# Kernel optimization log

Measured on AMD Instinct MI355X. Metric: run time of the kernel, lower is better.

The kernel has to match this reference:

```python
import jax, jax.numpy as jnp
import numpy as np

B, N, C, H = 2, 2048, 256, 8
HD = C // H
EPS = 1e-5


def _cdist(a, b):
    # a: (B,N,D), b: (B,M,D) -> (B,N,M) euclidean distance (torch.cdist p=2)
    d2 = (jnp.sum(a * a, -1)[:, :, None] + jnp.sum(b * b, -1)[:, None, :]
          - 2.0 * jnp.einsum('bnd,bmd->bnm', a, b))
    return jnp.sqrt(jnp.maximum(d2, 0.0))


def _ln(x, g, b):
    # LayerNorm over last axis
    m = jnp.mean(x, -1, keepdims=True)
    v = jnp.var(x, -1, keepdims=True)
    return (x - m) / jnp.sqrt(v + EPS) * g + b


def _conv1d(x, w, b=None):
    # 1x1 Conv1d: x (B,Cin,N), w (Cout,Cin)
    y = jnp.einsum('oc,bcn->bon', w, x)
    return y if b is None else y + b[:, None]


def setup_inputs() -> dict:
    key = jax.random.key(0)
    ks = jax.random.split(key, 32)
    s = 0.05
    inp = {
        'xyz_A': jax.random.normal(ks[0], (B, N, 3), jnp.float32),
        'featA': jax.random.normal(ks[1], (B, C, N), jnp.float32),
        'xyz_B': jax.random.normal(ks[2], (B, N, 3), jnp.float32),
        'featB': jax.random.normal(ks[3], (B, C, N), jnp.float32),
        # q/k/v projections (Conv1d 1x1)
        'qw': jax.random.normal(ks[4], (C, C), jnp.float32) * s,
        'qb': jnp.zeros((C,), jnp.float32),
        'kw': jax.random.normal(ks[5], (C, C), jnp.float32) * s,
        'kb': jnp.zeros((C,), jnp.float32),
        'vw': jax.random.normal(ks[6], (C, C), jnp.float32) * s,
        'vb': jnp.zeros((C,), jnp.float32),
        # spatial_bias_mlp: Conv2d(1,H/2,1,bias=False) -> BN2d(eval) -> ReLU -> Conv2d(H/2,H,1)
        'sbw1': jax.random.normal(ks[7], (H // 2,), jnp.float32) * s,
        'sbg': jnp.ones((H // 2,), jnp.float32),
        'sbb': jnp.zeros((H // 2,), jnp.float32),
        'sbm': jax.random.normal(ks[8], (H // 2,), jnp.float32) * 0.1,
        'sbv': jax.random.uniform(ks[9], (H // 2,), jnp.float32, 0.5, 1.5),
        'sbw2': jax.random.normal(ks[10], (H, H // 2), jnp.float32) * s,
        'sbb2': jnp.zeros((H,), jnp.float32),
        # dissimilarity projections
        'qdw': jax.random.normal(ks[11], (C, C), jnp.float32) * s,
        'qdb': jnp.zeros((C,), jnp.float32),
        'kdw': jax.random.normal(ks[12], (C, C), jnp.float32) * s,
        'kdb': jnp.zeros((C,), jnp.float32),
        # LayerNorms
        'lin_g': jnp.ones((C,), jnp.float32), 'lin_b': jnp.zeros((C,), jnp.float32),
        'lsim_g': jnp.ones((C,), jnp.float32), 'lsim_b': jnp.zeros((C,), jnp.float32),
        'ldis_g': jnp.ones((C,), jnp.float32), 'ldis_b': jnp.zeros((C,), jnp.float32),
        # fusion MLP: Conv1d(3C,2C,bias=False) -> BN1d(eval) -> ReLU -> Dropout(eval) -> Conv1d(2C,C)
        'fw1': jax.random.normal(ks[13], (2 * C, 3 * C), jnp.float32) * s,
        'fbg': jnp.ones((2 * C,), jnp.float32),
        'fbb': jnp.zeros((2 * C,), jnp.float32),
        'fbm': jax.random.normal(ks[14], (2 * C,), jnp.float32) * 0.1,
        'fbv': jax.random.uniform(ks[15], (2 * C,), jnp.float32, 0.5, 1.5),
        'fw2': jax.random.normal(ks[16], (C, 2 * C), jnp.float32) * s,
        'fb2': jnp.zeros((C,), jnp.float32),
    }
    return inp


def _forward(xyz_A, featA, xyz_B, featB, qw, qb, kw, kb, vw, vb,
             sbw1, sbg, sbb, sbm, sbv, sbw2, sbb2,
             qdw, qdb, kdw, kdb,
             lin_g, lin_b, lsim_g, lsim_b, ldis_g, ldis_b,
             fw1, fbg, fbb, fbm, fbv, fw2, fb2):
    # Pre-norm of featA over channels
    featA_norm = _ln(featA.transpose(0, 2, 1), lin_g, lin_b).transpose(0, 2, 1)  # (B,C,N)

    # Spatial bias: -cdist -> 1x1 conv (in_ch=1) -> BN(eval) -> ReLU -> 1x1 conv
    dist = _cdist(xyz_A, xyz_B)                                # (B,N,N)
    t = jnp.einsum('o,bnm->bonm', sbw1, -dist)                 # (B,H/2,N,N)
    t = (t - sbm[:, None, None]) / jnp.sqrt(sbv + EPS)[:, None, None]
    t = t * sbg[:, None, None] + sbb[:, None, None]
    t = jax.nn.relu(t)
    spatial_bias = jnp.einsum('oh,bhnm->bonm', sbw2, t) + sbb2[:, None, None]  # (B,H,N,N)

    # Similarity path
    q = _conv1d(featA_norm, qw, qb).reshape(B, H, HD, N).transpose(0, 1, 3, 2)  # (B,H,N,hd)
    k = _conv1d(featB, kw, kb).reshape(B, H, HD, N).transpose(0, 1, 3, 2)
    sim_scores = jnp.einsum('bhnd,bhmd->bhnm', q, k) / (HD ** 0.5) + spatial_bias

    # Dissimilarity path: feature cdist + spatial bias
    qd = _conv1d(featA_norm, qdw, qdb).transpose(0, 2, 1)      # (B,N,C)
    kd = _conv1d(featB, kdw, kdb).transpose(0, 2, 1)
    dissim_scores = _cdist(qd, kd)[:, None] + spatial_bias     # (B,H,N,N)

    sim_w = jax.nn.softmax(sim_scores, -1)
    dis_w = jax.nn.softmax(dissim_scores, -1)

    v = _conv1d(featB, vw, vb).reshape(B, H, HD, N).transpose(0, 1, 3, 2)       # (B,H,N,hd)
    ctx_sim = jnp.einsum('bhnm,bhmd->bhnd', sim_w, v).transpose(0, 1, 3, 2).reshape(B, C, N)
    ctx_sim = _ln(ctx_sim.transpose(0, 2, 1), lsim_g, lsim_b).transpose(0, 2, 1)
    ctx_dis = jnp.einsum('bhnm,bhmd->bhnd', dis_w, v).transpose(0, 1, 3, 2).reshape(B, C, N)
    ctx_dis = _ln(ctx_dis.transpose(0, 2, 1), ldis_g, ldis_b).transpose(0, 2, 1)

    fused = jnp.concatenate([featA_norm, ctx_sim, ctx_dis], axis=1)            # (B,3C,N)
    x = jnp.einsum('oc,bcn->bon', fw1, fused)
    x = (x - fbm[:, None]) / jnp.sqrt(fbv + EPS)[:, None] * fbg[:, None] + fbb[:, None]
    x = jax.nn.relu(x)  # Dropout is identity in eval mode
    out = _conv1d(x, fw2, fb2) + featA  # residual_proj is Identity (in==out)
    return out


def reference(xyz_A, featA, xyz_B, featB, qw, qb, kw, kb, vw, vb,
              sbw1, sbg, sbb, sbm, sbv, sbw2, sbb2,
              qdw, qdb, kdw, kdb,
              lin_g, lin_b, lsim_g, lsim_b, ldis_g, ldis_b,
              fw1, fbg, fbb, fbm, fbv, fw2, fb2):
    return _forward(xyz_A, featA, xyz_B, featB, qw, qb, kw, kb, vw, vb,
                    sbw1, sbg, sbb, sbm, sbv, sbw2, sbb2,
                    qdw, qdb, kdw, kdb,
                    lin_g, lin_b, lsim_g, lsim_b, ldis_g, ldis_b,
                    fw1, fbg, fbb, fbm, fbv, fw2, fb2)
```

## Files before the change

### kernel.cpp

```cpp
#include <hip/hip_runtime.h>

#define B_ 2
#define N_ 2048
#define C_ 256
#define H_ 8
#define HD_ 32
#define EPSf 1e-5f

typedef __bf16   bf16x8 __attribute__((ext_vector_type(8)));
typedef float    f32x4  __attribute__((ext_vector_type(4)));
typedef _Float16 f16x8  __attribute__((ext_vector_type(8)));
typedef _Float16 f16x4  __attribute__((ext_vector_type(4)));
typedef _Float16 f16x2  __attribute__((ext_vector_type(2)));

static constexpr size_t MB_ = 1024 * 1024;
static constexpr size_t OFF_FANT = 0;
static constexpr size_t OFF_FBT  = 2 * MB_;
static constexpr size_t OFF_QPK  = 4 * MB_;
static constexpr size_t OFF_KPK  = 6 * MB_;
static constexpr size_t OFF_VPK  = 8 * MB_;
static constexpr size_t OFF_QDT  = 10 * MB_;
static constexpr size_t OFF_KDT  = 12 * MB_;
static constexpr size_t OFF_QQ   = 14 * MB_;
static constexpr size_t OFF_KK   = 14 * MB_ + 16 * 1024;
static constexpr size_t OFF_FDH  = 14 * MB_ + 64 * 1024;
static constexpr size_t OFF_FSD  = 14 * MB_ + 64 * 1024;
static constexpr size_t OFF_CTXS = 31 * MB_;
static constexpr size_t OFF_CTXD = 35 * MB_;
static constexpr size_t OFF_CSLN = 39 * MB_;
static constexpr size_t OFF_CDLN = 41 * MB_;
static constexpr size_t OFF_X1T  = 43 * MB_;
static constexpr size_t WS_NEED  = 47 * MB_;
static constexpr size_t OFF2_PART  = 47 * MB_;
static constexpr size_t OFF2_STATM = 55 * MB_;
static constexpr size_t OFF2_STATL = 56 * MB_;
static constexpr size_t OFF2_CSLN  = 15 * MB_;
static constexpr size_t OFF2_CDLN  = 17 * MB_;
static constexpr size_t OFF2_X1T   = 19 * MB_;
static constexpr size_t WS_NEED2   = 63 * MB_;

__device__ __forceinline__ float rfl(float x){
  return __uint_as_float(__builtin_amdgcn_readfirstlane(__float_as_uint(x)));
}
__device__ __forceinline__ bf16x8 cvt8(const float* p){
  float4 a = *reinterpret_cast<const float4*>(p);
  float4 c = *reinterpret_cast<const float4*>(p + 4);
  bf16x8 r;
  r[0]=(__bf16)a.x; r[1]=(__bf16)a.y; r[2]=(__bf16)a.z; r[3]=(__bf16)a.w;
  r[4]=(__bf16)c.x; r[5]=(__bf16)c.y; r[6]=(__bf16)c.z; r[7]=(__bf16)c.w;
  return r;
}
__device__ __forceinline__ unsigned int packh2(float lo, float hi){
  f16x2 h; h[0] = (_Float16)lo; h[1] = (_Float16)hi;
  return __builtin_bit_cast(unsigned int, h);
}
__device__ __forceinline__ void unpackh2(unsigned int u, float& lo, float& hi){
  f16x2 h = __builtin_bit_cast(f16x2, u);
  lo = (float)h[0]; hi = (float)h[1];
}

__global__ __launch_bounds__(256) void lnA_pack(const float* __restrict__ featA,
    __bf16* __restrict__ fanT, const float* __restrict__ gam, const float* __restrict__ bet){
  int b = blockIdx.y, n0 = blockIdx.x * 32;
  int t = threadIdx.x, nl = t & 31, cg = t >> 5;
  __shared__ float tile[256][33];
  __shared__ float red1[8][32], red2[8][32], mus[32], rss[32];
  __shared__ float gsh[256], bsh[256];
  gsh[t] = gam[t]; bsh[t] = bet[t];
  #pragma unroll
  for (int i = 0; i < 32; i++){
    int c = cg * 32 + i;
    tile[c][nl] = featA[((size_t)(b * C_ + c)) * N_ + n0 + nl];
  }
  __syncthreads();
  float s1 = 0.f, s2 = 0.f;
  #pragma unroll
  for (int i = 0; i < 32; i++){
    float v = tile[cg * 32 + i][nl];
    s1 += v; s2 += v * v;
  }
  red1[cg][nl] = s1; red2[cg][nl] = s2;
  __syncthreads();
  if (t < 32){
    float a = 0.f, q = 0.f;
    #pragma unroll
    for (int i = 0; i < 8; i++){ a += red1[i][t]; q += red2[i][t]; }
    float m = a / (float)C_;
    mus[t] = m; rss[t] = rsqrtf(q / (float)C_ - m * m + EPSf);
  }
  __syncthreads();
  float mu = mus[nl], rs = rss[nl];
  size_t obase = ((size_t)(b * N_ + n0 + nl)) * C_;
  #pragma unroll
  for (int i = 0; i < 32; i++){
    int c = cg * 32 + i;
    fanT[obase + c] = (__bf16)((tile[c][nl] - mu) * rs * gsh[c] + bsh[c]);
  }
}

__global__ __launch_bounds__(256) void packT_kernel(const float* __restrict__ featB,
    __bf16* __restrict__ fbT){
  int b = blockIdx.z, c0 = blockIdx.y * 64, n0 = blockIdx.x * 64;
  int t = threadIdx.x;
  __shared__ float tile[64][65];
  int cl = t >> 6, nl = t & 63;
  #pragma unroll
  for (int i = 0; i < 16; i++)
    tile[i * 4 + cl][nl] = featB[((size_t)(b * C_ + c0 + i * 4 + cl)) * N_ + n0 + nl];
  __syncthreads();
  int nr = t >> 2, cc = (t & 3) * 16;
  alignas(16) __bf16 tmp[16];
  #pragma unroll
  for (int j = 0; j < 16; j++) tmp[j] = (__bf16)tile[cc + j][nr];
  size_t d = ((size_t)(b * N_ + n0 + nr)) * C_ + c0 + cc;
  *reinterpret_cast<uint4*>(&fbT[d])     = *reinterpret_cast<uint4*>(&tmp[0]);
  *reinterpret_cast<uint4*>(&fbT[d + 8]) = *reinterpret_cast<uint4*>(&tmp[8]);
}

__global__ __launch_bounds__(256) void proj_mfma(const __bf16* __restrict__ fanT,
    const __bf16* __restrict__ fbT, __bf16* __restrict__ wsh, int vfp16,
    const float* __restrict__ qw, const float* __restrict__ qb,
    const float* __restrict__ kw, const float* __restrict__ kb,
    const float* __restrict__ vw, const float* __restrict__ vb,
    const float* __restrict__ qdw, const float* __restrict__ qdb,
    const float* __restrict__ kdw, const float* __restrict__ kdb){
  const int p = blockIdx.z % 5, b = blockIdx.z / 5;
  const int t = threadIdx.x, w = t >> 6, lane = t & 63, ln = lane & 15, g = lane >> 4;
  const float *W, *bias;
  const __bf16* X;
  __bf16* Y;
  if (p == 0)      { W = qw;  bias = qb;  X = fanT; Y = wsh + (OFF_QPK - OFF_FANT) / 2; }
  else if (p == 1) { W = kw;  bias = kb;  X = fbT;  Y = wsh + (OFF_KPK - OFF_FANT) / 2; }
  else if (p == 2) { W = vw;  bias = vb;  X = fbT;  Y = wsh + (OFF_VPK - OFF_FANT) / 2; }
  else if (p == 3) { W = qdw; bias = qdb; X = fanT; Y = wsh + (OFF_QDT - OFF_FANT) / 2; }
  else             { W = kdw; bias = kdb; X = fbT;  Y = wsh + (OFF_KDT - OFF_FANT) / 2; }

  f32x4 acc[4];
  #pragma unroll
  for (int i = 0; i < 4; i++) acc[i] = (f32x4){0.f, 0.f, 0.f, 0.f};

  if (p != 2){
    const int n0w = blockIdx.x * 64 + w * 16, o0 = blockIdx.y * 64;
    #pragma unroll
    for (int ks = 0; ks < 8; ks++){
      bf16x8 af = *reinterpret_cast<const bf16x8*>(
          &X[((size_t)(b * N_ + n0w + ln)) * C_ + ks * 32 + g * 8]);
      #pragma unroll
      for (int ot = 0; ot < 4; ot++){
        bf16x8 bf = cvt8(&W[(size_t)(o0 + ot * 16 + ln) * C_ + ks * 32 + g * 8]);
        acc[ot] = __builtin_amdgcn_mfma_f32_16x16x32_bf16(af, bf, acc[ot], 0, 0, 0);
      }
    }
    const float inv = 0.17677669529663687f;
    #pragma unroll
    for (int ot = 0; ot < 4; ot++){
      int o = o0 + ot * 16 + ln;
      float bz = bias[o];
      #pragma unroll
      for (int r = 0; r < 4; r++){
        int n = n0w + g * 4 + r;
        float val = acc[ot][r] + bz;
        if (p == 0){
          val *= inv;
          Y[(((size_t)(b * H_ + (o >> 5))) * N_ + n) * HD_ + (o & 31)] = (__bf16)val;
        } else if (p == 1){
          Y[(((size_t)(b * H_ + (o >> 5))) * N_ + n) * HD_ + (o & 31)] = (__bf16)val;
        } else {
          Y[((size_t)(b * N_ + n)) * C_ + o] = (__bf16)val;
        }
      }
    }
  } else {
    const int o0w = blockIdx.y * 64 + w * 16, n0 = blockIdx.x * 64;
    #pragma unroll
    for (int ks = 0; ks < 8; ks++){
      bf16x8 af = cvt8(&W[(size_t)(o0w + ln) * C_ + ks * 32 + g * 8]);
      #pragma unroll
      for (int nt = 0; nt < 4; nt++){
        bf16x8 bf = *reinterpret_cast<const bf16x8*>(
            &X[((size_t)(b * N_ + n0 + nt * 16 + ln)) * C_ + ks * 32 + g * 8]);
        acc[nt] = __builtin_amdgcn_mfma_f32_16x16x32_bf16(af, bf, acc[nt], 0, 0, 0);
      }
    }
    float bz[4];
    #pragma unroll
    for (int r = 0; r < 4; r++) bz[r] = vb[o0w + g * 4 + r];
    #pragma unroll
    for (int nt = 0; nt < 4; nt++)
      #pragma unroll
      for (int r = 0; r < 4; r++){
        int o = o0w + g * 4 + r, n = n0 + nt * 16 + ln;
        size_t idx = ((size_t)(b * C_ + o)) * N_ + n;
        float val = acc[nt][r] + bz[r];
        if (vfp16) ((_Float16*)Y)[idx] = (_Float16)val;
        else       Y[idx] = (__bf16)val;
      }
  }
}

__global__ __launch_bounds__(256) void norms_b(const __bf16* __restrict__ qdT,
    const __bf16* __restrict__ kdT, float* __restrict__ qq, float* __restrict__ kk){
  int b = blockIdx.y, n = blockIdx.x * 64 + (threadIdx.x >> 2), part = threadIdx.x & 3;
  size_t base = ((size_t)(b * N_ + n)) * C_ + part * 64;
  float s1 = 0.f, s2 = 0.f;
  #pragma unroll
  for (int i = 0; i < 8; i++){
    bf16x8 a = *reinterpret_cast<const bf16x8*>(&qdT[base + i * 8]);
    bf16x8 d = *reinterpret_cast<const bf16x8*>(&kdT[base + i * 8]);
    #pragma unroll
    for (int j = 0; j < 8; j++){
      float fa = (float)a[j]; s1 += fa * fa;
      float fd = (float)d[j]; s2 += fd * fd;
    }
  }
  s1 += __shfl_xor(s1, 1); s1 += __shfl_xor(s1, 2);
  s2 += __shfl_xor(s2, 1); s2 += __shfl_xor(s2, 2);
  if (part == 0){ qq[b * N_ + n] = s1; kk[b * N_ + n] = s2; }
}

__global__ __launch_bounds__(256) void pairdist_mfma(const __bf16* __restrict__ qdT,
    const __bf16* __restrict__ kdT, const float* __restrict__ qq,
    const float* __restrict__ kk, const float* __restrict__ xyzA,
    const float* __restrict__ xyzB, unsigned int* __restrict__ fsd){
  const int t = threadIdx.x, w = t >> 6, lane = t & 63, ln = lane & 15, g = lane >> 4;
  const int b = blockIdx.z, n0 = blockIdx.y * 64, n0w = n0 + w * 16, m0 = blockIdx.x * 64;
  __shared__ float4 xa[64], xb[64];
  __shared__ unsigned int sbl[4][16][68];

  if (t < 64){
    const float* p = &xyzA[((size_t)(b * N_ + n0 + t)) * 3];
    xa[t] = make_float4(p[0], p[1], p[2], 0.f);
  } else if (t < 128){
    const float* p = &xyzB[((size_t)(b * N_ + m0 + t - 64)) * 3];
    xb[t - 64] = make_float4(p[0], p[1], p[2], 0.f);
  }
  bf16x8 qfr[8];
  #pragma unroll
  for (int ks = 0; ks < 8; ks++)
    qfr[ks] = *reinterpret_cast<const bf16x8*>(
        &qdT[((size_t)(b * N_ + n0w + ln)) * C_ + ks * 32 + g * 8]);
  float qqv[4];
  #pragma unroll
  for (int r = 0; r < 4; r++) qqv[r] = qq[b * N_ + n0w + g * 4 + r];
  __syncthreads();
  float4 xav[4];
  #pragma unroll
  for (int r = 0; r < 4; r++) xav[r] = xa[w * 16 + g * 4 + r];

  #pragma unroll
  for (int mt = 0; mt < 4; mt++){
    f32x4 a = (f32x4){0.f, 0.f, 0.f, 0.f};
    #pragma unroll
    for (int ks = 0; ks < 8; ks++){
      bf16x8 kfr = *reinterpret_cast<const bf16x8*>(
          &kdT[((size_t)(b * N_ + m0 + mt * 16 + ln)) * C_ + ks * 32 + g * 8]);
      a = __builtin_amdgcn_mfma_f32_16x16x32_bf16(qfr[ks], kfr, a, 0, 0, 0);
    }
    float kkv = kk[b * N_ + m0 + mt * 16 + ln];
    float4 xbv = xb[mt * 16 + ln];
    #pragma unroll
    for (int r = 0; r < 4; r++){
      float d2 = qqv[r] + kkv - 2.f * a[r];
      float fd = sqrtf(fmaxf(d2, 0.f));
      float dx = xav[r].x - xbv.x, dy = xav[r].y - xbv.y, dz = xav[r].z - xbv.z;
      float sd = sqrtf(dx * dx + dy * dy + dz * dz);
      sbl[w][g * 4 + r][mt * 16 + ln] = packh2(fd, sd);
    }
  }
  #pragma unroll
  for (int it = 0; it < 4; it++){
    int row = it * 4 + (lane >> 4), cq = lane & 15;
    uint4 v = *reinterpret_cast<const uint4*>(&sbl[w][row][cq * 4]);
    *reinterpret_cast<uint4*>(&fsd[((size_t)(b * N_ + n0w + row)) * N_ + m0 + cq * 4]) = v;
  }
}

struct TileRegs { uint4 fu[4]; bf16x8 kf[4]; };

__device__ __forceinline__ void load_tile(TileRegs& T, const __bf16* kbase,
    const unsigned int* fsdrow, int m0, int ln, int g){
  #pragma unroll
  for (int mt = 0; mt < 4; mt++){
    T.fu[mt] = *reinterpret_cast<const uint4*>(&fsdrow[m0 + mt * 16 + g * 4]);
    T.kf[mt] = *reinterpret_cast<const bf16x8*>(&kbase[(size_t)(m0 + mt * 16 + ln) * HD_ + g * 8]);
  }
}

__device__ __forceinline__ void compute_tile(const TileRegs& T,
    const _Float16* vbase, int m0, int ln, int g, bf16x8 qf,
    const float* Ac, const float* Bc, const float* W2h, float C0,
    f32x4* os, f32x4* od, float& ms, float& ls, float& md, float& ld){
  f32x4 sa[4];
  #pragma unroll
  for (int mt = 0; mt < 4; mt++){
    f32x4 z = (f32x4){0.f, 0.f, 0.f, 0.f};
    sa[mt] = __builtin_amdgcn_mfma_f32_16x16x32_bf16(T.kf[mt], qf, z, 0, 0, 0);
  }
  f16x4 vf[2][4];
  #pragma unroll
  for (int mt = 0; mt < 4; mt++)
    #pragma unroll
    for (int dt = 0; dt < 2; dt++)
      vf[dt][mt] = *reinterpret_cast<const f16x4*>(
          &vbase[(size_t)(dt * 16 + ln) * N_ + m0 + mt * 16 + g * 4]);
  f32x4 dvv[4];
  float mxs = -3e38f, mxd = -3e38f;
  #pragma unroll
  for (int mt = 0; mt < 4; mt++){
    #pragma unroll
    for (int r = 0; r < 4; r++){
      unsigned int uu = (r == 0) ? T.fu[mt].x : (r == 1) ? T.fu[mt].y
                      : (r == 2) ? T.fu[mt].z : T.fu[mt].w;
      float fd, sd;
      unpackh2(uu, fd, sd);
      float u0 = fmaxf(fmaf(Ac[0], sd, Bc[0]), 0.f);
      float u1 = fmaxf(fmaf(Ac[1], sd, Bc[1]), 0.f);
      float u2 = fmaxf(fmaf(Ac[2], sd, Bc[2]), 0.f);
      float u3 = fmaxf(fmaf(Ac[3], sd, Bc[3]), 0.f);
      float bias = C0 + W2h[0] * u0 + W2h[1] * u1 + W2h[2] * u2 + W2h[3] * u3;
      float s = sa[mt][r] + bias;
      float d = fd + bias;
      sa[mt][r] = s; dvv[mt][r] = d;
      mxs = fmaxf(mxs, s); mxd = fmaxf(mxd, d);
    }
  }
  mxs = fmaxf(mxs, __shfl_xor(mxs, 16)); mxs = fmaxf(mxs, __shfl_xor(mxs, 32));
  mxd = fmaxf(mxd, __shfl_xor(mxd, 16)); mxd = fmaxf(mxd, __shfl_xor(mxd, 32));
  float nms = fmaxf(ms, mxs), als = __expf(ms - nms);
  float nmd = fmaxf(md, mxd), ald = __expf(md - nmd);
  f16x4 pAs[4], pAd[4];
  float pss = 0.f, psd = 0.f;
  #pragma unroll
  for (int mt = 0; mt < 4; mt++)
    #pragma unroll
    for (int r = 0; r < 4; r++){
      float pv = __expf(sa[mt][r] - nms); pss += pv; pAs[mt][r] = (_Float16)pv;
      float qv = __expf(dvv[mt][r] - nmd); psd += qv; pAd[mt][r] = (_Float16)qv;
    }
  pss += __shfl_xor(pss, 16); pss += __shfl_xor(pss, 32);
  psd += __shfl_xor(psd, 16); psd += __shfl_xor(psd, 32);
  ls = ls * als + pss; ms = nms;
  ld = ld * ald + psd; md = nmd;
  float alsr[4], aldr[4];
  #pragma unroll
  for (int r = 0; r < 4; r++){
    alsr[r] = __shfl(als, g * 4 + r);
    aldr[r] = __shfl(ald, g * 4 + r);
  }
  #pragma unroll
  for (int dt = 0; dt < 2; dt++)
    #pragma unroll
    for (int r = 0; r < 4; r++){ os[dt][r] *= alsr[r]; od[dt][r] *= aldr[r]; }
  #pragma unroll
  for (int mt = 0; mt < 4; mt++)
    #pragma unroll
    for (int dt = 0; dt < 2; dt++){
      os[dt] = __builtin_amdgcn_mfma_f32_16x16x16f16(pAs[mt], vf[dt][mt], os[dt], 0, 0, 0);
      od[dt] = __builtin_amdgcn_mfma_f32_16x16x16f16(pAd[mt], vf[dt][mt], od[dt], 0, 0, 0);
    }
}

__global__ __launch_bounds__(256) void dual_attn3(
    const __bf16* __restrict__ qpk, const __bf16* __restrict__ kpk,
    const _Float16* __restrict__ vph, const unsigned int* __restrict__ fsd,
    const float* __restrict__ sbw1, const float* __restrict__ sbg, const float* __restrict__ sbb,
    const float* __restrict__ sbm, const float* __restrict__ sbv,
    const float* __restrict__ sbw2, const float* __restrict__ sbb2,
    _Float16* __restrict__ partO, float* __restrict__ statM, float* __restrict__ statL){
  const int t = threadIdx.x, w = t >> 6, lane = t & 63, ln = lane & 15, g = lane >> 4;
  const int h = blockIdx.y;
  const int b = blockIdx.z >> 1, split = blockIdx.z & 1;
  const int nbase = blockIdx.x * 64 + w * 16;
  const int n = nbase + ln;
  const int mstart = split * (N_ / 2);

  float Ac[4], Bc[4], W2h[4];
  #pragma unroll
  for (int j = 0; j < 4; j++){
    float rs = rsqrtf(sbv[j] + EPSf);
    Ac[j]  = rfl(-sbw1[j] * rs * sbg[j]);
    Bc[j]  = rfl(-sbm[j] * rs * sbg[j] + sbb[j]);
    W2h[j] = rfl(sbw2[h * 4 + j]);
  }
  float C0 = rfl(sbb2[h]);

  bf16x8 qf = *reinterpret_cast<const bf16x8*>(
      &qpk[(((size_t)(b * H_ + h)) * N_ + n) * HD_ + g * 8]);
  const unsigned int* fsdrow = &fsd[((size_t)(b * N_ + n)) * N_];
  const __bf16* kbase = &kpk[(((size_t)(b * H_ + h)) * N_) * HD_];
  const _Float16* vbase = &vph[((size_t)(b * C_ + h * HD_)) * N_];

  f32x4 os[2], od[2];
  #pragma unroll
  for (int i = 0; i < 2; i++){ os[i] = (f32x4){0.f,0.f,0.f,0.f}; od[i] = (f32x4){0.f,0.f,0.f,0.f}; }
  float ms = -3e38f, ls = 0.f, md = -3e38f, ld = 0.f;

  TileRegs TA, TB;
  load_tile(TA, kbase, fsdrow, mstart, ln, g);
  for (int i = 0; i < 16; i += 2){
    int m0 = mstart + i * 64;
    load_tile(TB, kbase, fsdrow, m0 + 64, ln, g);
    compute_tile(TA, vbase, m0, ln, g, qf, Ac, Bc, W2h, C0, os, od, ms, ls, md, ld);
    if (i + 2 < 16) load_tile(TA, kbase, fsdrow, m0 + 128, ln, g);
    compute_tile(TB, vbase, m0 + 64, ln, g, qf, Ac, Bc, W2h, C0, os, od, ms, ls, md, ld);
  }

  float is = 1.f / ls, idd = 1.f / ld;
  float isr[4], idr[4];
  #pragma unroll
  for (int r = 0; r < 4; r++){
    isr[r] = __shfl(is, g * 4 + r);
    idr[r] = __shfl(idd, g * 4 + r);
  }
  #pragma unroll
  for (int dt = 0; dt < 2; dt++)
    #pragma unroll
    for (int r = 0; r < 4; r++){
      int nn = nbase + g * 4 + r;
      int ch = h * HD_ + dt * 16 + ln;
      size_t p0 = (((size_t)(0 * 2 + split) * B_ + b) * N_ + nn) * C_ + ch;
      size_t p1 = (((size_t)(2 + split) * B_ + b) * N_ + nn) * C_ + ch;
      partO[p0] = (_Float16)(os[dt][r] * isr[r]);
      partO[p1] = (_Float16)(od[dt][r] * idr[r]);
    }
  if (lane < 16){
    int nn = nbase + lane;
    size_t s0 = (((size_t)(0 * 2 + split) * B_ + b) * H_ + h) * N_ + nn;
    size_t s1 = (((size_t)(2 + split) * B_ + b) * H_ + h) * N_ + nn;
    statM[s0] = ms; statL[s0] = ls;
    statM[s1] = md; statL[s1] = ld;
  }
}

__global__ __launch_bounds__(256) void combine_ln(
    const _Float16* __restrict__ partO, const float* __restrict__ statM,
    const float* __restrict__ statL, __bf16* __restrict__ csLN, __bf16* __restrict__ cdLN,
    const float* __restrict__ lsg, const float* __restrict__ lsb,
    const float* __restrict__ ldg, const float* __restrict__ ldb){
  const int path = blockIdx.y;
  const int w = threadIdx.x >> 6, lane = threadIdx.x & 63;
  const size_t row = (size_t)blockIdx.x * 4 + w;
  const int b = (int)(row >> 11), n = (int)(row & (N_ - 1));
  const int h = lane >> 3;
  const float* gg = path ? ldg : lsg;
  const float* bb = path ? ldb : lsb;
  __bf16* dst = path ? cdLN : csLN;

  size_t pb0 = (((size_t)(path * 2 + 0) * B_ + b) * N_ + n) * C_ + lane * 4;
  size_t pb1 = (((size_t)(path * 2 + 1) * B_ + b) * N_ + n) * C_ + lane * 4;
  f16x4 p0 = *reinterpret_cast<const f16x4*>(&partO[pb0]);
  f16x4 p1 = *reinterpret_cast<const f16x4*>(&partO[pb1]);
  size_t sb0 = (((size_t)(path * 2 + 0) * B_ + b) * H_ + h) * N_ + n;
  size_t sb1 = (((size_t)(path * 2 + 1) * B_ + b) * H_ + h) * N_ + n;
  float m0 = statM[sb0], l0 = statL[sb0];
  float m1 = statM[sb1], l1 = statL[sb1];
  float M = fmaxf(m0, m1);
  float w0 = l0 * __expf(m0 - M), w1 = l1 * __expf(m1 - M);
  float inv = 1.f / (w0 + w1);
  float o[4];
  #pragma unroll
  for (int j = 0; j < 4; j++)
    o[j] = (w0 * (float)p0[j] + w1 * (float)p1[j]) * inv;

  float s1 = o[0] + o[1] + o[2] + o[3];
  float s2 = o[0]*o[0] + o[1]*o[1] + o[2]*o[2] + o[3]*o[3];
  #pragma unroll
  for (int off = 1; off < 64; off <<= 1){
    s1 += __shfl_xor(s1, off);
    s2 += __shfl_xor(s2, off);
  }
  float mu = s1 / (float)C_;
  float rs = rsqrtf(s2 / (float)C_ - mu * mu + EPSf);
  float4 g4 = *reinterpret_cast<const float4*>(&gg[lane * 4]);
  float4 b4 = *reinterpret_cast<const float4*>(&bb[lane * 4]);
  alignas(8) __bf16 o4[4];
  o4[0] = (__bf16)((o[0] - mu) * rs * g4.x + b4.x);
  o4[1] = (__bf16)((o[1] - mu) * rs * g4.y + b4.y);
  o4[2] = (__bf16)((o[2] - mu) * rs * g4.z + b4.z);
  o4[3] = (__bf16)((o[3] - mu) * rs * g4.w + b4.w);
  *reinterpret_cast<uint2*>(&dst[row * C_ + lane * 4]) = *reinterpret_cast<uint2*>(o4);
}

__global__ __launch_bounds__(256) void fdist_mfma(const __bf16* __restrict__ qdT,
    const __bf16* __restrict__ kdT, const float* __restrict__ qq,
    const float* __restrict__ kk, _Float16* __restrict__ fdh){
  const int t = threadIdx.x, w = t >> 6, lane = t & 63, ln = lane & 15, g = lane >> 4;
  const int b = blockIdx.z, n0 = blockIdx.y * 64 + w * 16, m0 = blockIdx.x * 64;
  __shared__ _Float16 sbl[4][16][68];

  bf16x8 qfr[8];
  #pragma unroll
  for (int ks = 0; ks < 8; ks++)
    qfr[ks] = *reinterpret_cast<const bf16x8*>(
        &qdT[((size_t)(b * N_ + n0 + ln)) * C_ + ks * 32 + g * 8]);
  float qqv[4];
  #pragma unroll
  for (int r = 0; r < 4; r++) qqv[r] = qq[b * N_ + n0 + g * 4 + r];

  #pragma unroll
  for (int mt = 0; mt < 4; mt++){
    f32x4 a = (f32x4){0.f, 0.f, 0.f, 0.f};
    #pragma unroll
    for (int ks = 0; ks < 8; ks++){
      bf16x8 kfr = *reinterpret_cast<const bf16x8*>(
          &kdT[((size_t)(b * N_ + m0 + mt * 16 + ln)) * C_ + ks * 32 + g * 8]);
      a = __builtin_amdgcn_mfma_f32_16x16x32_bf16(qfr[ks], kfr, a, 0, 0, 0);
    }
    float kkv = kk[b * N_ + m0 + mt * 16 + ln];
    #pragma unroll
    for (int r = 0; r < 4; r++){
      float d2 = qqv[r] + kkv - 2.f * a[r];
      sbl[w][g * 4 + r][mt * 16 + ln] = (_Float16)sqrtf(fmaxf(d2, 0.f));
    }
  }
  __syncthreads();
  #pragma unroll
  for (int it = 0; it < 8; it++){
    int row = (lane >> 5) + it * 2, colu = lane & 31;
    unsigned int u = *reinterpret_cast<const unsigned int*>(&sbl[w][row][colu * 2]);
    *reinterpret_cast<unsigned int*>(&fdh[((size_t)(b * N_ + n0 + row)) * N_ + m0 + colu * 2]) = u;
  }
}

__global__ __launch_bounds__(256) void dual_attn(
    const __bf16* __restrict__ qpk, const __bf16* __restrict__ kpk, const __bf16* __restrict__ vpk,
    const _Float16* __restrict__ fdh,
    const float* __restrict__ xyzA, const float* __restrict__ xyzB,
    const float* __restrict__ sbw1, const float* __restrict__ sbg, const float* __restrict__ sbb,
    const float* __restrict__ sbm, const float* __restrict__ sbv,
    const float* __restrict__ sbw2, const float* __restrict__ sbb2,
    float* __restrict__ ctxsT, float* __restrict__ ctxdT){
  const int t = threadIdx.x, w = t >> 6, lane = t & 63, ln = lane & 15, g = lane >> 4;
  const int h = blockIdx.y, b = blockIdx.z;
  const int nbase = blockIdx.x * 64 + w * 16;
  const int n = nbase + ln;

  float Ac[4], Bc[4], W2h[4];
  #pragma unroll
  for (int j = 0; j < 4; j++){
    float rs = rsqrtf(sbv[j] + EPSf);
    Ac[j]  = rfl(-sbw1[j] * rs * sbg[j]);
    Bc[j]  = rfl(-sbm[j] * rs * sbg[j] + sbb[j]);
    W2h[j] = rfl(sbw2[h * 4 + j]);
  }
  float C0 = rfl(sbb2[h]);

  bf16x8 qf = *reinterpret_cast<const bf16x8*>(
      &qpk[(((size_t)(b * H_ + h)) * N_ + n) * HD_ + g * 8]);
  float ax = xyzA[((size_t)(b * N_ + n)) * 3 + 0];
  float ay = xyzA[((size_t)(b * N_ + n)) * 3 + 1];
  float az = xyzA[((size_t)(b * N_ + n)) * 3 + 2];
  const _Float16* fdrow = &fdh[((size_t)(b * N_ + n)) * N_];

  f32x4 os[2], od[2];
  #pragma unroll
  for (int i = 0; i < 2; i++){ os[i] = (f32x4){0.f,0.f,0.f,0.f}; od[i] = (f32x4){0.f,0.f,0.f,0.f}; }
  float ms = -3e38f, ls = 0.f, md = -3e38f, ld = 0.f;

  __shared__ __align__(16) float ss[4][16][68];
  __shared__ float4 xbb[4][64];

  for (int m0 = 0; m0 < N_; m0 += 64){
    __syncthreads();
    {
      const float* xp = &xyzB[((size_t)(b * N_ + m0 + lane)) * 3];
      xbb[w][lane] = make_float4(xp[0], xp[1], xp[2], 0.f);
    }
    f32x4 sa[4];
    #pragma unroll
    for (int i = 0; i < 4; i++) sa[i] = (f32x4){0.f, 0.f, 0.f, 0.f};
    #pragma unroll
    for (int mt = 0; mt < 4; mt++){
      bf16x8 kf = *reinterpret_cast<const bf16x8*>(
          &kpk[(((size_t)(b * H_ + h)) * N_ + m0 + mt * 16 + ln) * HD_ + g * 8]);
      sa[mt] = __builtin_amdgcn_mfma_f32_16x16x32_bf16(qf, kf, sa[mt], 0, 0, 0);
    }
    #pragma unroll
    for (int mt = 0; mt < 4; mt++)
      #pragma unroll
      for (int r = 0; r < 4; r++)
        ss[w][g * 4 + r][mt * 16 + ln] = sa[mt][r];
    __syncthreads();

    #pragma unroll
    for (int kh = 0; kh < 2; kh++){
      float s8[8], d8[8];
      {
        float4 A4 = *reinterpret_cast<const float4*>(&ss[w][ln][kh * 32 + g * 8]);
        float4 B4 = *reinterpret_cast<const float4*>(&ss[w][ln][kh * 32 + g * 8 + 4]);
        s8[0]=A4.x; s8[1]=A4.y; s8[2]=A4.z; s8[3]=A4.w;
        s8[4]=B4.x; s8[5]=B4.y; s8[6]=B4.z; s8[7]=B4.w;
      }
      f16x8 fv = *reinterpret_cast<const f16x8*>(&fdrow[m0 + kh * 32 + g * 8]);
      float mxs = -3e38f, mxd = -3e38f;
      #pragma unroll
      for (int j = 0; j < 8; j++){
        float4 xk = xbb[w][kh * 32 + g * 8 + j];
        float dx = ax - xk.x, dy = ay - xk.y, dz = az - xk.z;
        float sd = sqrtf(dx * dx + dy * dy + dz * dz);
        float bias = C0;
        #pragma unroll
        for (int u = 0; u < 4; u++)
          bias += W2h[u] * fmaxf(fmaf(Ac[u], sd, Bc[u]), 0.f);
        s8[j] += bias;
        d8[j] = (float)fv[j] + bias;
        mxs = fmaxf(mxs, s8[j]);
        mxd = fmaxf(mxd, d8[j]);
      }
      mxs = fmaxf(mxs, __shfl_xor(mxs, 16)); mxs = fmaxf(mxs, __shfl_xor(mxs, 32));
      mxd = fmaxf(mxd, __shfl_xor(mxd, 16)); mxd = fmaxf(mxd, __shfl_xor(mxd, 32));
      float nms = fmaxf(ms, mxs), als = __expf(ms - nms);
      float nmd = fmaxf(md, mxd), ald = __expf(md - nmd);
      float pss = 0.f, psd = 0.f;
      bf16x8 pfs, pfd;
      #pragma unroll
      for (int j = 0; j < 8; j++){
        float pv = __expf(s8[j] - nms); pss += pv; pfs[j] = (__bf16)pv;
        float qv = __expf(d8[j] - nmd); psd += qv; pfd[j] = (__bf16)qv;
      }
      pss += __shfl_xor(pss, 16); pss += __shfl_xor(pss, 32);
      psd += __shfl_xor(psd, 16); psd += __shfl_xor(psd, 32);
      ls = ls * als + pss; ms = nms;
      ld = ld * ald + psd; md = nmd;
      os[0] *= als; os[1] *= als; od[0] *= ald; od[1] *= ald;
      #pragma unroll
      for (int dt = 0; dt < 2; dt++){
        bf16x8 vf = *reinterpret_cast<const bf16x8*>(
            &vpk[((size_t)(b * C_ + h * HD_ + dt * 16 + ln)) * N_ + m0 + kh * 32 + g * 8]);
        os[dt] = __builtin_amdgcn_mfma_f32_16x16x32_bf16(vf, pfs, os[dt], 0, 0, 0);
        od[dt] = __builtin_amdgcn_mfma_f32_16x16x32_bf16(vf, pfd, od[dt], 0, 0, 0);
      }
    }
  }
  float is = 1.f / ls, idv = 1.f / ld;
  #pragma unroll
  for (int dt = 0; dt < 2; dt++)
    #pragma unroll
    for (int r = 0; r < 4; r++){
      int ch = h * HD_ + dt * 16 + g * 4 + r;
      size_t base = ((size_t)(b * N_ + n)) * C_ + ch;
      ctxsT[base] = os[dt][r] * is;
      ctxdT[base] = od[dt][r] * idv;
    }
}

__global__ __launch_bounds__(256) void ln_ctx(const float* __restrict__ ctxsT,
    const float* __restrict__ ctxdT, __bf16* __restrict__ csLN, __bf16* __restrict__ cdLN,
    const float* __restrict__ lsg, const float* __restrict__ lsb,
    const float* __restrict__ ldg, const float* __restrict__ ldb){
  const float* src = blockIdx.y ? ctxdT : ctxsT;
  __bf16* dst = blockIdx.y ? cdLN : csLN;
  const float* gg = blockIdx.y ? ldg : lsg;
  const float* bb = blockIdx.y ? ldb : lsb;
  int w = threadIdx.x >> 6, lane = threadIdx.x & 63;
  size_t row = (size_t)blockIdx.x * 4 + w;
  float4 v = *reinterpret_cast<const float4*>(&src[row * C_ + lane * 4]);
  float s1 = v.x + v.y + v.z + v.w;
  float s2 = v.x * v.x + v.y * v.y + v.z * v.z + v.w * v.w;
  #pragma unroll
  for (int off = 1; off < 64; off <<= 1){
    s1 += __shfl_xor(s1, off);
    s2 += __shfl_xor(s2, off);
  }
  float m = s1 / (float)C_;
  float rs = rsqrtf(s2 / (float)C_ - m * m + EPSf);
  float4 g4 = *reinterpret_cast<const float4*>(&gg[lane * 4]);
  float4 b4 = *reinterpret_cast<const float4*>(&bb[lane * 4]);
  alignas(8) __bf16 o4[4];
  o4[0] = (__bf16)((v.x - m) * rs * g4.x + b4.x);
  o4[1] = (__bf16)((v.y - m) * rs * g4.y + b4.y);
  o4[2] = (__bf16)((v.z - m) * rs * g4.z + b4.z);
  o4[3] = (__bf16)((v.w - m) * rs * g4.w + b4.w);
  *reinterpret_cast<uint2*>(&dst[row * C_ + lane * 4]) = *reinterpret_cast<uint2*>(o4);
}

__global__ __launch_bounds__(256) void fusion1_mfma(const __bf16* __restrict__ fanT,
    const __bf16* __restrict__ csLN, const __bf16* __restrict__ cdLN,
    __bf16* __restrict__ X1T, const float* __restrict__ fw1,
    const float* __restrict__ fbg, const float* __restrict__ fbb,
    const float* __restrict__ fbm, const float* __restrict__ fbv){
  const int t = threadIdx.x, w = t >> 6, lane = t & 63, ln = lane & 15, g = lane >> 4;
  const int b = blockIdx.z, o0 = blockIdx.y * 64, n0w = blockIdx.x * 64 + w * 16;
  f32x4 acc[4];
  #pragma unroll
  for (int i = 0; i < 4; i++) acc[i] = (f32x4){0.f, 0.f, 0.f, 0.f};
  const __bf16* segs[3] = {fanT, csLN, cdLN};
  #pragma unroll
  for (int ks = 0; ks < 24; ks++){
    const __bf16* base = segs[ks >> 3];
    int coff = (ks & 7) * 32 + g * 8;
    bf16x8 af = *reinterpret_cast<const bf16x8*>(
        &base[((size_t)(b * N_ + n0w + ln)) * C_ + coff]);
    #pragma unroll
    for (int ot = 0; ot < 4; ot++){
      bf16x8 bf = cvt8(&fw1[(size_t)(o0 + ot * 16 + ln) * (3 * C_) + ks * 32 + g * 8]);
      acc[ot] = __builtin_amdgcn_mfma_f32_16x16x32_bf16(af, bf, acc[ot], 0, 0, 0);
    }
  }
  #pragma unroll
  for (int ot = 0; ot < 4; ot++){
    int o = o0 + ot * 16 + ln;
    float mn = fbm[o], rs = rsqrtf(fbv[o] + EPSf), gg = fbg[o], be = fbb[o];
    #pragma unroll
    for (int r = 0; r < 4; r++){
      int n = n0w + g * 4 + r;
      float x = (acc[ot][r] - mn) * rs * gg + be;
      X1T[((size_t)(b * N_ + n)) * (2 * C_) + o] = (__bf16)fmaxf(x, 0.f);
    }
  }
}

__global__ __launch_bounds__(256) void fusion2_mfma(const __bf16* __restrict__ X1T,
    const float* __restrict__ fw2, const float* __restrict__ fb2,
    const float* __restrict__ featA, float* __restrict__ out){
  const int t = threadIdx.x, w = t >> 6, lane = t & 63, ln = lane & 15, g = lane >> 4;
  const int b = blockIdx.z, o0w = blockIdx.y * 64 + w * 16, n0 = blockIdx.x * 64;
  f32x4 acc[4];
  #pragma unroll
  for (int i = 0; i < 4; i++) acc[i] = (f32x4){0.f, 0.f, 0.f, 0.f};
  #pragma unroll
  for (int ks = 0; ks < 16; ks++){
    bf16x8 af = cvt8(&fw2[(size_t)(o0w + ln) * (2 * C_) + ks * 32 + g * 8]);
    #pragma unroll
    for (int nt = 0; nt < 4; nt++){
      bf16x8 bf = *reinterpret_cast<const bf16x8*>(
          &X1T[((size_t)(b * N_ + n0 + nt * 16 + ln)) * (2 * C_) + ks * 32 + g * 8]);
      acc[nt] = __builtin_amdgcn_mfma_f32_16x16x32_bf16(af, bf, acc[nt], 0, 0, 0);
    }
  }
  float bz[4];
  #pragma unroll
  for (int r = 0; r < 4; r++) bz[r] = fb2[o0w + g * 4 + r];
  #pragma unroll
  for (int nt = 0; nt < 4; nt++)
    #pragma unroll
    for (int r = 0; r < 4; r++){
      int o = o0w + g * 4 + r, n = n0 + nt * 16 + ln;
      size_t oi = ((size_t)(b * C_ + o)) * N_ + n;
      out[oi] = acc[nt][r] + bz[r] + featA[oi];
    }
}

extern "C" void kernel_launch(void* const* d_in, const int* in_sizes, int n_in,
                              void* d_out, int out_size, void* d_ws, size_t ws_size,
                              hipStream_t stream){
  (void)in_sizes; (void)n_in; (void)out_size;
  if (ws_size < WS_NEED) return;

  const float* xyzA  = (const float*)d_in[0];
  const float* featA = (const float*)d_in[1];
  const float* xyzB  = (const float*)d_in[2];
  const float* featB = (const float*)d_in[3];
  const float* qw  = (const float*)d_in[4];   const float* qb  = (const float*)d_in[5];
  const float* kw  = (const float*)d_in[6];   const float* kb  = (const float*)d_in[7];
  const float* vw  = (const float*)d_in[8];   const float* vb  = (const float*)d_in[9];
  const float* sbw1= (const float*)d_in[10];  const float* sbg = (const float*)d_in[11];
  const float* sbb = (const float*)d_in[12];  const float* sbm = (const float*)d_in[13];
  const float* sbv = (const float*)d_in[14];  const float* sbw2= (const float*)d_in[15];
  const float* sbb2= (const float*)d_in[16];
  const float* qdw = (const float*)d_in[17];  const float* qdb = (const float*)d_in[18];
  const float* kdw = (const float*)d_in[19];  const float* kdb = (const float*)d_in[20];
  const float* ling= (const float*)d_in[21];  const float* linb= (const float*)d_in[22];
  const float* lsg = (const float*)d_in[23];  const float* lsb = (const float*)d_in[24];
  const float* ldg = (const float*)d_in[25];  const float* ldb = (const float*)d_in[26];
  const float* fw1 = (const float*)d_in[27];  const float* fbg = (const float*)d_in[28];
  const float* fbb = (const float*)d_in[29];  const float* fbm = (const float*)d_in[30];
  const float* fbv = (const float*)d_in[31];  const float* fw2 = (const float*)d_in[32];
  const float* fb2 = (const float*)d_in[33];

  char* ws = (char*)d_ws;
  __bf16*   fanT = (__bf16*)(ws + OFF_FANT);
  __bf16*   fbT  = (__bf16*)(ws + OFF_FBT);
  __bf16*   qpk  = (__bf16*)(ws + OFF_QPK);
  __bf16*   kpk  = (__bf16*)(ws + OFF_KPK);
  __bf16*   qdT  = (__bf16*)(ws + OFF_QDT);
  __bf16*   kdT  = (__bf16*)(ws + OFF_KDT);
  float*    qq   = (float*)(ws + OFF_QQ);
  float*    kk   = (float*)(ws + OFF_KK);
  float*    out  = (float*)d_out;

  bool big = (ws_size >= WS_NEED2);

  lnA_pack<<<dim3(N_ / 32, B_), 256, 0, stream>>>(featA, fanT, ling, linb);
  packT_kernel<<<dim3(N_ / 64, C_ / 64, B_), 256, 0, stream>>>(featB, fbT);
  proj_mfma<<<dim3(N_ / 64, C_ / 64, 5 * B_), 256, 0, stream>>>(
      fanT, fbT, fanT, big ? 1 : 0, qw, qb, kw, kb, vw, vb, qdw, qdb, kdw, kdb);
  norms_b<<<dim3(N_ / 64, B_), 256, 0, stream>>>(qdT, kdT, qq, kk);

  if (big){
    _Float16*     vph  = (_Float16*)(ws + OFF_VPK);
    unsigned int* fsd  = (unsigned int*)(ws + OFF_FSD);
    _Float16* partO = (_Float16*)(ws + OFF2_PART);
    float*    statM = (float*)(ws + OFF2_STATM);
    float*    statL = (float*)(ws + OFF2_STATL);
    __bf16*   csLN  = (__bf16*)(ws + OFF2_CSLN);
    __bf16*   cdLN  = (__bf16*)(ws + OFF2_CDLN);
    __bf16*   X1T   = (__bf16*)(ws + OFF2_X1T);
    pairdist_mfma<<<dim3(N_ / 64, N_ / 64, B_), 256, 0, stream>>>(
        qdT, kdT, qq, kk, xyzA, xyzB, fsd);
    dual_attn3<<<dim3(N_ / 64, H_, B_ * 2), 256, 0, stream>>>(
        qpk, kpk, vph, fsd, sbw1, sbg, sbb, sbm, sbv, sbw2, sbb2,
        partO, statM, statL);
    combine_ln<<<dim3(B_ * N_ / 4, 2), 256, 0, stream>>>(
        partO, statM, statL, csLN, cdLN, lsg, lsb, ldg, ldb);
    fusion1_mfma<<<dim3(N_ / 64, (2 * C_) / 64, B_), 256, 0, stream>>>(
        fanT, csLN, cdLN, X1T, fw1, fbg, fbb, fbm, fbv);
    fusion2_mfma<<<dim3(N_ / 64, C_ / 64, B_), 256, 0, stream>>>(
        X1T, fw2, fb2, featA, out);
  } else {
    __bf16*   vpk  = (__bf16*)(ws + OFF_VPK);
    _Float16* fdh  = (_Float16*)(ws + OFF_FDH);
    float*  ctxsT = (float*)(ws + OFF_CTXS);
    float*  ctxdT = (float*)(ws + OFF_CTXD);
    __bf16* csLN  = (__bf16*)(ws + OFF_CSLN);
    __bf16* cdLN  = (__bf16*)(ws + OFF_CDLN);
    __bf16* X1T   = (__bf16*)(ws + OFF_X1T);
    fdist_mfma<<<dim3(N_ / 64, N_ / 64, B_), 256, 0, stream>>>(qdT, kdT, qq, kk, fdh);
    dual_attn<<<dim3(N_ / 64, H_, B_), 256, 0, stream>>>(
        qpk, kpk, vpk, fdh, xyzA, xyzB,
        sbw1, sbg, sbb, sbm, sbv, sbw2, sbb2, ctxsT, ctxdT);
    ln_ctx<<<dim3(B_ * N_ / 4, 2), 256, 0, stream>>>(
        ctxsT, ctxdT, csLN, cdLN, lsg, lsb, ldg, ldb);
    fusion1_mfma<<<dim3(N_ / 64, (2 * C_) / 64, B_), 256, 0, stream>>>(
        fanT, csLN, cdLN, X1T, fw1, fbg, fbb, fbm, fbv);
    fusion2_mfma<<<dim3(N_ / 64, C_ / 64, B_), 256, 0, stream>>>(
        X1T, fw2, fb2, featA, out);
  }
}
```

Measured before the change: 270.9 us.

## Use exp2 softmax with lazy rescaling and merge prep kernels

Folds log2(e) into the query scale, the feature distance and the spatial-bias weights so the online softmax can use the hardware exp2 directly. The running max and rescale are updated only when some row max grows past a threshold, and the per-tile row-sum shuffles are deferred to the end. LayerNorm-pack and transpose-pack are merged into one launch, and the small-workspace fallback path is removed. The threshold-skipped rescale lets exponent values grow up to 2^8 before fp16 packing, which risks precision loss. Dropping the fallback assumes the large workspace is always available.

```diff
diff --git a/kernel.cpp b/kernel.cpp
--- a/kernel.cpp
+++ b/kernel.cpp
@@ -6,10 +6,11 @@
 #define H_ 8
 #define HD_ 32
 #define EPSf 1e-5f
+#define LOG2E 1.4426950408889634f
+#define THRv 8.0f
 
 typedef __bf16   bf16x8 __attribute__((ext_vector_type(8)));
 typedef float    f32x4  __attribute__((ext_vector_type(4)));
-typedef _Float16 f16x8  __attribute__((ext_vector_type(8)));
 typedef _Float16 f16x4  __attribute__((ext_vector_type(4)));
 typedef _Float16 f16x2  __attribute__((ext_vector_type(2)));
 
@@ -23,25 +24,19 @@
 static constexpr size_t OFF_KDT  = 12 * MB_;
 static constexpr size_t OFF_QQ   = 14 * MB_;
 static constexpr size_t OFF_KK   = 14 * MB_ + 16 * 1024;
-static constexpr size_t OFF_FDH  = 14 * MB_ + 64 * 1024;
 static constexpr size_t OFF_FSD  = 14 * MB_ + 64 * 1024;
-static constexpr size_t OFF_CTXS = 31 * MB_;
-static constexpr size_t OFF_CTXD = 35 * MB_;
-static constexpr size_t OFF_CSLN = 39 * MB_;
-static constexpr size_t OFF_CDLN = 41 * MB_;
-static constexpr size_t OFF_X1T  = 43 * MB_;
-static constexpr size_t WS_NEED  = 47 * MB_;
-static constexpr size_t OFF2_PART  = 47 * MB_;
-static constexpr size_t OFF2_STATM = 55 * MB_;
-static constexpr size_t OFF2_STATL = 56 * MB_;
-static constexpr size_t OFF2_CSLN  = 15 * MB_;
-static constexpr size_t OFF2_CDLN  = 17 * MB_;
-static constexpr size_t OFF2_X1T   = 19 * MB_;
-static constexpr size_t WS_NEED2   = 63 * MB_;
+static constexpr size_t OFF_PART  = 47 * MB_;
+static constexpr size_t OFF_STATM = 55 * MB_;
+static constexpr size_t OFF_STATL = 56 * MB_;
+static constexpr size_t OFF_CSLN  = 15 * MB_;
+static constexpr size_t OFF_CDLN  = 17 * MB_;
+static constexpr size_t OFF_X1T   = 19 * MB_;
+static constexpr size_t WS_NEED   = 63 * MB_;
 
 __device__ __forceinline__ float rfl(float x){
   return __uint_as_float(__builtin_amdgcn_readfirstlane(__float_as_uint(x)));
 }
+__device__ __forceinline__ float fexp2(float x){ return __builtin_amdgcn_exp2f(x); }
 __device__ __forceinline__ bf16x8 cvt8(const float* p){
   float4 a = *reinterpret_cast<const float4*>(p);
   float4 c = *reinterpret_cast<const float4*>(p + 4);
@@ -58,67 +53,81 @@
   f16x2 h = __builtin_bit_cast(f16x2, u);
   lo = (float)h[0]; hi = (float)h[1];
 }
-
-__global__ __launch_bounds__(256) void lnA_pack(const float* __restrict__ featA,
-    __bf16* __restrict__ fanT, const float* __restrict__ gam, const float* __restrict__ bet){
-  int b = blockIdx.y, n0 = blockIdx.x * 32;
-  int t = threadIdx.x, nl = t & 31, cg = t >> 5;
-  __shared__ float tile[256][33];
-  __shared__ float red1[8][32], red2[8][32], mus[32], rss[32];
-  __shared__ float gsh[256], bsh[256];
-  gsh[t] = gam[t]; bsh[t] = bet[t];
-  #pragma unroll
-  for (int i = 0; i < 32; i++){
-    int c = cg * 32 + i;
-    tile[c][nl] = featA[((size_t)(b * C_ + c)) * N_ + n0 + nl];
-  }
-  __syncthreads();
-  float s1 = 0.f, s2 = 0.f;
-  #pragma unroll
-  for (int i = 0; i < 32; i++){
-    float v = tile[cg * 32 + i][nl];
-    s1 += v; s2 += v * v;
-  }
-  red1[cg][nl] = s1; red2[cg][nl] = s2;
-  __syncthreads();
-  if (t < 32){
-    float a = 0.f, q = 0.f;
-    #pragma unroll
-    for (int i = 0; i < 8; i++){ a += red1[i][t]; q += red2[i][t]; }
-    float m = a / (float)C_;
-    mus[t] = m; rss[t] = rsqrtf(q / (float)C_ - m * m + EPSf);
-  }
-  __syncthreads();
-  float mu = mus[nl], rs = rss[nl];
-  size_t obase = ((size_t)(b * N_ + n0 + nl)) * C_;
-  #pragma unroll
-  for (int i = 0; i < 32; i++){
-    int c = cg * 32 + i;
-    fanT[obase + c] = (__bf16)((tile[c][nl] - mu) * rs * gsh[c] + bsh[c]);
-  }
-}
-
-__global__ __launch_bounds__(256) void packT_kernel(const float* __restrict__ featB,
-    __bf16* __restrict__ fbT){
-  int b = blockIdx.z, c0 = blockIdx.y * 64, n0 = blockIdx.x * 64;
+__device__ __forceinline__ f16x4 pack4(float a, float b, float c, float d){
+  auto lo = __builtin_amdgcn_cvt_pkrtz(a, b);
+  auto hi = __builtin_amdgcn_cvt_pkrtz(c, d);
+  unsigned long long u = (unsigned long long)__builtin_bit_cast(unsigned int, lo)
+      | ((unsigned long long)__builtin_bit_cast(unsigned int, hi) << 32);
+  return __builtin_bit_cast(f16x4, u);
+}
+
+__global__ __launch_bounds__(256) void prep_kernel(const float* __restrict__ featA,
+    const float* __restrict__ featB, __bf16* __restrict__ fanT, __bf16* __restrict__ fbT,
+    const float* __restrict__ gam, const float* __restrict__ bet){
+  int b = blockIdx.y;
   int t = threadIdx.x;
-  __shared__ float tile[64][65];
-  int cl = t >> 6, nl = t & 63;
-  #pragma unroll
-  for (int i = 0; i < 16; i++)
-    tile[i * 4 + cl][nl] = featB[((size_t)(b * C_ + c0 + i * 4 + cl)) * N_ + n0 + nl];
-  __syncthreads();
-  int nr = t >> 2, cc = (t & 3) * 16;
-  alignas(16) __bf16 tmp[16];
-  #pragma unroll
-  for (int j = 0; j < 16; j++) tmp[j] = (__bf16)tile[cc + j][nr];
-  size_t d = ((size_t)(b * N_ + n0 + nr)) * C_ + c0 + cc;
-  *reinterpret_cast<uint4*>(&fbT[d])     = *reinterpret_cast<uint4*>(&tmp[0]);
-  *reinterpret_cast<uint4*>(&fbT[d + 8]) = *reinterpret_cast<uint4*>(&tmp[8]);
+  __shared__ float sh[9536];
+  if (blockIdx.x < 64){
+    int n0 = blockIdx.x * 32;
+    int nl = t & 31, cg = t >> 5;
+    float* tile = sh;
+    float* red1 = sh + 8448;
+    float* red2 = red1 + 256;
+    float* mus  = red2 + 256;
+    float* rss  = mus + 32;
+    float* gsh  = rss + 32;
+    float* bsh  = gsh + 256;
+    gsh[t] = gam[t]; bsh[t] = bet[t];
+    #pragma unroll
+    for (int i = 0; i < 32; i++){
+      int c = cg * 32 + i;
+      tile[c * 33 + nl] = featA[((size_t)(b * C_ + c)) * N_ + n0 + nl];
+    }
+    __syncthreads();
+    float s1 = 0.f, s2 = 0.f;
+    #pragma unroll
+    for (int i = 0; i < 32; i++){
+      float v = tile[(cg * 32 + i) * 33 + nl];
+      s1 += v; s2 += v * v;
+    }
+    red1[cg * 32 + nl] = s1; red2[cg * 32 + nl] = s2;
+    __syncthreads();
+    if (t < 32){
+      float a = 0.f, q = 0.f;
+      #pragma unroll
+      for (int i = 0; i < 8; i++){ a += red1[i * 32 + t]; q += red2[i * 32 + t]; }
+      float m = a / (float)C_;
+      mus[t] = m; rss[t] = rsqrtf(q / (float)C_ - m * m + EPSf);
+    }
+    __syncthreads();
+    float mu = mus[nl], rs = rss[nl];
+    size_t obase = ((size_t)(b * N_ + n0 + nl)) * C_;
+    #pragma unroll
+    for (int i = 0; i < 32; i++){
+      int c = cg * 32 + i;
+      fanT[obase + c] = (__bf16)((tile[c * 33 + nl] - mu) * rs * gsh[c] + bsh[c]);
+    }
+  } else {
+    int idx = blockIdx.x - 64;
+    int n0 = (idx & 31) * 64, c0 = (idx >> 5) * 64;
+    float* tile = sh;
+    int cl = t >> 6, nl = t & 63;
+    #pragma unroll
+    for (int i = 0; i < 16; i++)
+      tile[(i * 4 + cl) * 65 + nl] = featB[((size_t)(b * C_ + c0 + i * 4 + cl)) * N_ + n0 + nl];
+    __syncthreads();
+    int nr = t >> 2, cc = (t & 3) * 16;
+    alignas(16) __bf16 tmp[16];
+    #pragma unroll
+    for (int j = 0; j < 16; j++) tmp[j] = (__bf16)tile[(cc + j) * 65 + nr];
+    size_t d = ((size_t)(b * N_ + n0 + nr)) * C_ + c0 + cc;
+    *reinterpret_cast<uint4*>(&fbT[d])     = *reinterpret_cast<uint4*>(&tmp[0]);
+    *reinterpret_cast<uint4*>(&fbT[d + 8]) = *reinterpret_cast<uint4*>(&tmp[8]);
+  }
 }
 
 __global__ __launch_bounds__(256) void proj_mfma(const __bf16* __restrict__ fanT,
-    const __bf16* __restrict__ fbT, __bf16* __restrict__ wsh, int vfp16,
+    const __bf16* __restrict__ fbT, __bf16* __restrict__ wsh,
     const float* __restrict__ qw, const float* __restrict__ qb,
     const float* __restrict__ kw, const float* __restrict__ kb,
     const float* __restrict__ vw, const float* __restrict__ vb,
@@ -151,7 +160,7 @@
         acc[ot] = __builtin_amdgcn_mfma_f32_16x16x32_bf16(af, bf, acc[ot], 0, 0, 0);
       }
     }
-    const float inv = 0.17677669529663687f;
+    const float inv = 0.17677669529663687f * LOG2E;
     #pragma unroll
     for (int ot = 0; ot < 4; ot++){
       int o = o0 + ot * 16 + ln;
@@ -191,9 +200,7 @@
       for (int r = 0; r < 4; r++){
         int o = o0w + g * 4 + r, n = n0 + nt * 16 + ln;
         size_t idx = ((size_t)(b * C_ + o)) * N_ + n;
-        float val = acc[nt][r] + bz[r];
-        if (vfp16) ((_Float16*)Y)[idx] = (_Float16)val;
-        else       Y[idx] = (__bf16)val;
+        ((_Float16*)Y)[idx] = (_Float16)(acc[nt][r] + bz[r]);
       }
   }
 }
@@ -261,7 +268,7 @@
     #pragma unroll
     for (int r = 0; r < 4; r++){
       float d2 = qqv[r] + kkv - 2.f * a[r];
-      float fd = sqrtf(fmaxf(d2, 0.f));
+      float fd = sqrtf(fmaxf(d2, 0.f)) * LOG2E;
       float dx = xav[r].x - xbv.x, dy = xav[r].y - xbv.y, dz = xav[r].z - xbv.z;
       float sd = sqrtf(dx * dx + dy * dy + dz * dz);
       sbl[w][g * 4 + r][mt * 16 + ln] = packh2(fd, sd);
@@ -286,10 +293,10 @@
   }
 }
 
-__device__ __forceinline__ void compute_tile(const TileRegs& T,
+__device__ __forceinline__ void compute_tile4(const TileRegs& T,
     const _Float16* vbase, int m0, int ln, int g, bf16x8 qf,
     const float* Ac, const float* Bc, const float* W2h, float C0,
-    f32x4* os, f32x4* od, float& ms, float& ls, float& md, float& ld){
+    f32x4* os, f32x4* od, float& ms, float& lps, float& md, float& lpd){
   f32x4 sa[4];
   #pragma unroll
   for (int mt = 0; mt < 4; mt++){
@@ -311,46 +318,57 @@
     for (int r = 0; r < 4; r++){
       unsigned int uu = (r == 0) ? T.fu[mt].x : (r == 1) ? T.fu[mt].y
                       : (r == 2) ? T.fu[mt].z : T.fu[mt].w;
-      float fd, sd;
-      unpackh2(uu, fd, sd);
+      float fdl, sd;
+      unpackh2(uu, fdl, sd);
       float u0 = fmaxf(fmaf(Ac[0], sd, Bc[0]), 0.f);
       float u1 = fmaxf(fmaf(Ac[1], sd, Bc[1]), 0.f);
       float u2 = fmaxf(fmaf(Ac[2], sd, Bc[2]), 0.f);
       float u3 = fmaxf(fmaf(Ac[3], sd, Bc[3]), 0.f);
-      float bias = C0 + W2h[0] * u0 + W2h[1] * u1 + W2h[2] * u2 + W2h[3] * u3;
+      float bias = fmaf(W2h[0], u0, fmaf(W2h[1], u1, fmaf(W2h[2], u2, fmaf(W2h[3], u3, C0))));
       float s = sa[mt][r] + bias;
-      float d = fd + bias;
+      float d = fdl + bias;
       sa[mt][r] = s; dvv[mt][r] = d;
       mxs = fmaxf(mxs, s); mxd = fmaxf(mxd, d);
     }
   }
-  mxs = fmaxf(mxs, __shfl_xor(mxs, 16)); mxs = fmaxf(mxs, __shfl_xor(mxs, 32));
-  mxd = fmaxf(mxd, __shfl_xor(mxd, 16)); mxd = fmaxf(mxd, __shfl_xor(mxd, 32));
-  float nms = fmaxf(ms, mxs), als = __expf(ms - nms);
-  float nmd = fmaxf(md, mxd), ald = __expf(md - nmd);
+  if (!__all(mxs <= ms + THRv)){
+    float mr = fmaxf(mxs, __shfl_xor(mxs, 16));
+    mr = fmaxf(mr, __shfl_xor(mr, 32));
+    float nms = fmaxf(ms, mr);
+    float als = fexp2(ms - nms);
+    ms = nms; lps *= als;
+    float a0 = __shfl(als, g * 4 + 0), a1 = __shfl(als, g * 4 + 1);
+    float a2 = __shfl(als, g * 4 + 2), a3 = __shfl(als, g * 4 + 3);
+    #pragma unroll
+    for (int dt = 0; dt < 2; dt++){
+      os[dt][0] *= a0; os[dt][1] *= a1; os[dt][2] *= a2; os[dt][3] *= a3;
+    }
+  }
+  if (!__all(mxd <= md + THRv)){
+    float mr = fmaxf(mxd, __shfl_xor(mxd, 16));
+    mr = fmaxf(mr, __shfl_xor(mr, 32));
+    float nmd = fmaxf(md, mr);
+    float ald = fexp2(md - nmd);
+    md = nmd; lpd *= ald;
+    float a0 = __shfl(ald, g * 4 + 0), a1 = __shfl(ald, g * 4 + 1);
+    float a2 = __shfl(ald, g * 4 + 2), a3 = __shfl(ald, g * 4 + 3);
+    #pragma unroll
+    for (int dt = 0; dt < 2; dt++){
+      od[dt][0] *= a0; od[dt][1] *= a1; od[dt][2] *= a2; od[dt][3] *= a3;
+    }
+  }
   f16x4 pAs[4], pAd[4];
-  float pss = 0.f, psd = 0.f;
-  #pragma unroll
-  for (int mt = 0; mt < 4; mt++)
-    #pragma unroll
-    for (int r = 0; r < 4; r++){
-      float pv = __expf(sa[mt][r] - nms); pss += pv; pAs[mt][r] = (_Float16)pv;
-      float qv = __expf(dvv[mt][r] - nmd); psd += qv; pAd[mt][r] = (_Float16)qv;
-    }
-  pss += __shfl_xor(pss, 16); pss += __shfl_xor(pss, 32);
-  psd += __shfl_xor(psd, 16); psd += __shfl_xor(psd, 32);
-  ls = ls * als + pss; ms = nms;
-  ld = ld * ald + psd; md = nmd;
-  float alsr[4], aldr[4];
-  #pragma unroll
-  for (int r = 0; r < 4; r++){
-    alsr[r] = __shfl(als, g * 4 + r);
-    aldr[r] = __shfl(ald, g * 4 + r);
-  }
-  #pragma unroll
-  for (int dt = 0; dt < 2; dt++)
-    #pragma unroll
-    for (int r = 0; r < 4; r++){ os[dt][r] *= alsr[r]; od[dt][r] *= aldr[r]; }
+  #pragma unroll
+  for (int mt = 0; mt < 4; mt++){
+    float p0 = fexp2(sa[mt][0] - ms), p1 = fexp2(sa[mt][1] - ms);
+    float p2 = fexp2(sa[mt][2] - ms), p3 = fexp2(sa[mt][3] - ms);
+    lps += (p0 + p1) + (p2 + p3);
+    pAs[mt] = pack4(p0, p1, p2, p3);
+    float q0 = fexp2(dvv[mt][0] - md), q1 = fexp2(dvv[mt][1] - md);
+    float q2 = fexp2(dvv[mt][2] - md), q3 = fexp2(dvv[mt][3] - md);
+    lpd += (q0 + q1) + (q2 + q3);
+    pAd[mt] = pack4(q0, q1, q2, q3);
+  }
   #pragma unroll
   for (int mt = 0; mt < 4; mt++)
     #pragma unroll
@@ -360,7 +378,7 @@
     }
 }
 
-__global__ __launch_bounds__(256) void dual_attn3(
+__global__ __launch_bounds__(256) void dual_attn4(
     const __bf16* __restrict__ qpk, const __bf16* __restrict__ kpk,
     const _Float16* __restrict__ vph, const unsigned int* __restrict__ fsd,
     const float* __restrict__ sbw1, const float* __restrict__ sbg, const float* __restrict__ sbb,
@@ -380,9 +398,9 @@
     float rs = rsqrtf(sbv[j] + EPSf);
     Ac[j]  = rfl(-sbw1[j] * rs * sbg[j]);
     Bc[j]  = rfl(-sbm[j] * rs * sbg[j] + sbb[j]);
-    W2h[j] = rfl(sbw2[h * 4 + j]);
-  }
-  float C0 = rfl(sbb2[h]);
+    W2h[j] = rfl(sbw2[h * 4 + j]) * LOG2E;
+  }
+  float C0 = rfl(sbb2[h]) * LOG2E;
 
   bf16x8 qf = *reinterpret_cast<const bf16x8*>(
       &qpk[(((size_t)(b * H_ + h)) * N_ + n) * HD_ + g * 8]);
@@ -393,19 +411,21 @@
   f32x4 os[2], od[2];
   #pragma unroll
   for (int i = 0; i < 2; i++){ os[i] = (f32x4){0.f,0.f,0.f,0.f}; od[i] = (f32x4){0.f,0.f,0.f,0.f}; }
-  float ms = -3e38f, ls = 0.f, md = -3e38f, ld = 0.f;
+  float ms = -3e38f, lps = 0.f, md = -3e38f, lpd = 0.f;
 
   TileRegs TA, TB;
   load_tile(TA, kbase, fsdrow, mstart, ln, g);
   for (int i = 0; i < 16; i += 2){
     int m0 = mstart + i * 64;
     load_tile(TB, kbase, fsdrow, m0 + 64, ln, g);
-    compute_tile(TA, vbase, m0, ln, g, qf, Ac, Bc, W2h, C0, os, od, ms, ls, md, ld);
+    compute_tile4(TA, vbase, m0, ln, g, qf, Ac, Bc, W2h, C0, os, od, ms, lps, md, lpd);
     if (i + 2 < 16) load_tile(TA, kbase, fsdrow, m0 + 128, ln, g);
-    compute_tile(TB, vbase, m0 + 64, ln, g, qf, Ac, Bc, W2h, C0, os, od, ms, ls, md, ld);
-  }
-
-  float is = 1.f / ls, idd = 1.f / ld;
+    compute_tile4(TB, vbase, m0 + 64, ln, g, qf, Ac, Bc, W2h, C0, os, od, ms, lps, md, lpd);
+  }
+
+  lps += __shfl_xor(lps, 16); lps += __shfl_xor(lps, 32);
+  lpd += __shfl_xor(lpd, 16); lpd += __shfl_xor(lpd, 32);
+  float is = 1.f / lps, idd = 1.f / lpd;
   float isr[4], idr[4];
   #pragma unroll
   for (int r = 0; r < 4; r++){
@@ -427,8 +447,8 @@
     int nn = nbase + lane;
     size_t s0 = (((size_t)(0 * 2 + split) * B_ + b) * H_ + h) * N_ + nn;
     size_t s1 = (((size_t)(2 + split) * B_ + b) * H_ + h) * N_ + nn;
-    statM[s0] = ms; statL[s0] = ls;
-    statM[s1] = md; statL[s1] = ld;
+    statM[s0] = ms; statL[s0] = lps;
+    statM[s1] = md; statL[s1] = lpd;
   }
 }
 
@@ -455,7 +475,7 @@
   float m0 = statM[sb0], l0 = statL[sb0];
   float m1 = statM[sb1], l1 = statL[sb1];
   float M = fmaxf(m0, m1);
-  float w0 = l0 * __expf(m0 - M), w1 = l1 * __expf(m1 - M);
+  float w0 = l0 * fexp2(m0 - M), w1 = l1 * fexp2(m1 - M);
   float inv = 1.f / (w0 + w1);
   float o[4];
   #pragma unroll
@@ -478,199 +498,6 @@
   o4[1] = (__bf16)((o[1] - mu) * rs * g4.y + b4.y);
   o4[2] = (__bf16)((o[2] - mu) * rs * g4.z + b4.z);
   o4[3] = (__bf16)((o[3] - mu) * rs * g4.w + b4.w);
-  *reinterpret_cast<uint2*>(&dst[row * C_ + lane * 4]) = *reinterpret_cast<uint2*>(o4);
-}
-
-__global__ __launch_bounds__(256) void fdist_mfma(const __bf16* __restrict__ qdT,
-    const __bf16* __restrict__ kdT, const float* __restrict__ qq,
-    const float* __restrict__ kk, _Float16* __restrict__ fdh){
-  const int t = threadIdx.x, w = t >> 6, lane = t & 63, ln = lane & 15, g = lane >> 4;
-  const int b = blockIdx.z, n0 = blockIdx.y * 64 + w * 16, m0 = blockIdx.x * 64;
-  __shared__ _Float16 sbl[4][16][68];
-
-  bf16x8 qfr[8];
-  #pragma unroll
-  for (int ks = 0; ks < 8; ks++)
-    qfr[ks] = *reinterpret_cast<const bf16x8*>(
-        &qdT[((size_t)(b * N_ + n0 + ln)) * C_ + ks * 32 + g * 8]);
-  float qqv[4];
-  #pragma unroll
-  for (int r = 0; r < 4; r++) qqv[r] = qq[b * N_ + n0 + g * 4 + r];
-
-  #pragma unroll
-  for (int mt = 0; mt < 4; mt++){
-    f32x4 a = (f32x4){0.f, 0.f, 0.f, 0.f};
-    #pragma unroll
-    for (int ks = 0; ks < 8; ks++){
-      bf16x8 kfr = *reinterpret_cast<const bf16x8*>(
-          &kdT[((size_t)(b * N_ + m0 + mt * 16 + ln)) * C_ + ks * 32 + g * 8]);
-      a = __builtin_amdgcn_mfma_f32_16x16x32_bf16(qfr[ks], kfr, a, 0, 0, 0);
-    }
-    float kkv = kk[b * N_ + m0 + mt * 16 + ln];
-    #pragma unroll
-    for (int r = 0; r < 4; r++){
-      float d2 = qqv[r] + kkv - 2.f * a[r];
-      sbl[w][g * 4 + r][mt * 16 + ln] = (_Float16)sqrtf(fmaxf(d2, 0.f));
-    }
-  }
-  __syncthreads();
-  #pragma unroll
-  for (int it = 0; it < 8; it++){
-    int row = (lane >> 5) + it * 2, colu = lane & 31;
-    unsigned int u = *reinterpret_cast<const unsigned int*>(&sbl[w][row][colu * 2]);
-    *reinterpret_cast<unsigned int*>(&fdh[((size_t)(b * N_ + n0 + row)) * N_ + m0 + colu * 2]) = u;
-  }
-}
-
-__global__ __launch_bounds__(256) void dual_attn(
-    const __bf16* __restrict__ qpk, const __bf16* __restrict__ kpk, const __bf16* __restrict__ vpk,
-    const _Float16* __restrict__ fdh,
-    const float* __restrict__ xyzA, const float* __restrict__ xyzB,
-    const float* __restrict__ sbw1, const float* __restrict__ sbg, const float* __restrict__ sbb,
-    const float* __restrict__ sbm, const float* __restrict__ sbv,
-    const float* __restrict__ sbw2, const float* __restrict__ sbb2,
-    float* __restrict__ ctxsT, float* __restrict__ ctxdT){
-  const int t = threadIdx.x, w = t >> 6, lane = t & 63, ln = lane & 15, g = lane >> 4;
-  const int h = blockIdx.y, b = blockIdx.z;
-  const int nbase = blockIdx.x * 64 + w * 16;
-  const int n = nbase + ln;
-
-  float Ac[4], Bc[4], W2h[4];
-  #pragma unroll
-  for (int j = 0; j < 4; j++){
-    float rs = rsqrtf(sbv[j] + EPSf);
-    Ac[j]  = rfl(-sbw1[j] * rs * sbg[j]);
-    Bc[j]  = rfl(-sbm[j] * rs * sbg[j] + sbb[j]);
-    W2h[j] = rfl(sbw2[h * 4 + j]);
-  }
-  float C0 = rfl(sbb2[h]);
-
-  bf16x8 qf = *reinterpret_cast<const bf16x8*>(
-      &qpk[(((size_t)(b * H_ + h)) * N_ + n) * HD_ + g * 8]);
-  float ax = xyzA[((size_t)(b * N_ + n)) * 3 + 0];
-  float ay = xyzA[((size_t)(b * N_ + n)) * 3 + 1];
-  float az = xyzA[((size_t)(b * N_ + n)) * 3 + 2];
-  const _Float16* fdrow = &fdh[((size_t)(b * N_ + n)) * N_];
-
-  f32x4 os[2], od[2];
-  #pragma unroll
-  for (int i = 0; i < 2; i++){ os[i] = (f32x4){0.f,0.f,0.f,0.f}; od[i] = (f32x4){0.f,0.f,0.f,0.f}; }
-  float ms = -3e38f, ls = 0.f, md = -3e38f, ld = 0.f;
-
-  __shared__ __align__(16) float ss[4][16][68];
-  __shared__ float4 xbb[4][64];
-
-  for (int m0 = 0; m0 < N_; m0 += 64){
-    __syncthreads();
-    {
-      const float* xp = &xyzB[((size_t)(b * N_ + m0 + lane)) * 3];
-      xbb[w][lane] = make_float4(xp[0], xp[1], xp[2], 0.f);
-    }
-    f32x4 sa[4];
-    #pragma unroll
-    for (int i = 0; i < 4; i++) sa[i] = (f32x4){0.f, 0.f, 0.f, 0.f};
-    #pragma unroll
-    for (int mt = 0; mt < 4; mt++){
-      bf16x8 kf = *reinterpret_cast<const bf16x8*>(
-          &kpk[(((size_t)(b * H_ + h)) * N_ + m0 + mt * 16 + ln) * HD_ + g * 8]);
-      sa[mt] = __builtin_amdgcn_mfma_f32_16x16x32_bf16(qf, kf, sa[mt], 0, 0, 0);
-    }
-    #pragma unroll
-    for (int mt = 0; mt < 4; mt++)
-      #pragma unroll
-      for (int r = 0; r < 4; r++)
-        ss[w][g * 4 + r][mt * 16 + ln] = sa[mt][r];
-    __syncthreads();
-
-    #pragma unroll
-    for (int kh = 0; kh < 2; kh++){
-      float s8[8], d8[8];
-      {
-        float4 A4 = *reinterpret_cast<const float4*>(&ss[w][ln][kh * 32 + g * 8]);
-        float4 B4 = *reinterpret_cast<const float4*>(&ss[w][ln][kh * 32 + g * 8 + 4]);
-        s8[0]=A4.x; s8[1]=A4.y; s8[2]=A4.z; s8[3]=A4.w;
-        s8[4]=B4.x; s8[5]=B4.y; s8[6]=B4.z; s8[7]=B4.w;
-      }
-      f16x8 fv = *reinterpret_cast<const f16x8*>(&fdrow[m0 + kh * 32 + g * 8]);
-      float mxs = -3e38f, mxd = -3e38f;
-      #pragma unroll
-      for (int j = 0; j < 8; j++){
-        float4 xk = xbb[w][kh * 32 + g * 8 + j];
-        float dx = ax - xk.x, dy = ay - xk.y, dz = az - xk.z;
-        float sd = sqrtf(dx * dx + dy * dy + dz * dz);
-        float bias = C0;
-        #pragma unroll
-        for (int u = 0; u < 4; u++)
-          bias += W2h[u] * fmaxf(fmaf(Ac[u], sd, Bc[u]), 0.f);
-        s8[j] += bias;
-        d8[j] = (float)fv[j] + bias;
-        mxs = fmaxf(mxs, s8[j]);
-        mxd = fmaxf(mxd, d8[j]);
-      }
-      mxs = fmaxf(mxs, __shfl_xor(mxs, 16)); mxs = fmaxf(mxs, __shfl_xor(mxs, 32));
-      mxd = fmaxf(mxd, __shfl_xor(mxd, 16)); mxd = fmaxf(mxd, __shfl_xor(mxd, 32));
-      float nms = fmaxf(ms, mxs), als = __expf(ms - nms);
-      float nmd = fmaxf(md, mxd), ald = __expf(md - nmd);
-      float pss = 0.f, psd = 0.f;
-      bf16x8 pfs, pfd;
-      #pragma unroll
-      for (int j = 0; j < 8; j++){
-        float pv = __expf(s8[j] - nms); pss += pv; pfs[j] = (__bf16)pv;
-        float qv = __expf(d8[j] - nmd); psd += qv; pfd[j] = (__bf16)qv;
-      }
-      pss += __shfl_xor(pss, 16); pss += __shfl_xor(pss, 32);
-      psd += __shfl_xor(psd, 16); psd += __shfl_xor(psd, 32);
-      ls = ls * als + pss; ms = nms;
-      ld = ld * ald + psd; md = nmd;
-      os[0] *= als; os[1] *= als; od[0] *= ald; od[1] *= ald;
-      #pragma unroll
-      for (int dt = 0; dt < 2; dt++){
-        bf16x8 vf = *reinterpret_cast<const bf16x8*>(
-            &vpk[((size_t)(b * C_ + h * HD_ + dt * 16 + ln)) * N_ + m0 + kh * 32 + g * 8]);
-        os[dt] = __builtin_amdgcn_mfma_f32_16x16x32_bf16(vf, pfs, os[dt], 0, 0, 0);
-        od[dt] = __builtin_amdgcn_mfma_f32_16x16x32_bf16(vf, pfd, od[dt], 0, 0, 0);
-      }
-    }
-  }
-  float is = 1.f / ls, idv = 1.f / ld;
-  #pragma unroll
-  for (int dt = 0; dt < 2; dt++)
-    #pragma unroll
-    for (int r = 0; r < 4; r++){
-      int ch = h * HD_ + dt * 16 + g * 4 + r;
-      size_t base = ((size_t)(b * N_ + n)) * C_ + ch;
-      ctxsT[base] = os[dt][r] * is;
-      ctxdT[base] = od[dt][r] * idv;
-    }
-}
-
-__global__ __launch_bounds__(256) void ln_ctx(const float* __restrict__ ctxsT,
-    const float* __restrict__ ctxdT, __bf16* __restrict__ csLN, __bf16* __restrict__ cdLN,
-    const float* __restrict__ lsg, const float* __restrict__ lsb,
-    const float* __restrict__ ldg, const float* __restrict__ ldb){
-  const float* src = blockIdx.y ? ctxdT : ctxsT;
-  __bf16* dst = blockIdx.y ? cdLN : csLN;
-  const float* gg = blockIdx.y ? ldg : lsg;
-  const float* bb = blockIdx.y ? ldb : lsb;
-  int w = threadIdx.x >> 6, lane = threadIdx.x & 63;
-  size_t row = (size_t)blockIdx.x * 4 + w;
-  float4 v = *reinterpret_cast<const float4*>(&src[row * C_ + lane * 4]);
-  float s1 = v.x + v.y + v.z + v.w;
-  float s2 = v.x * v.x + v.y * v.y + v.z * v.z + v.w * v.w;
-  #pragma unroll
-  for (int off = 1; off < 64; off <<= 1){
-    s1 += __shfl_xor(s1, off);
-    s2 += __shfl_xor(s2, off);
-  }
-  float m = s1 / (float)C_;
-  float rs = rsqrtf(s2 / (float)C_ - m * m + EPSf);
-  float4 g4 = *reinterpret_cast<const float4*>(&gg[lane * 4]);
-  float4 b4 = *reinterpret_cast<const float4*>(&bb[lane * 4]);
-  alignas(8) __bf16 o4[4];
-  o4[0] = (__bf16)((v.x - m) * rs * g4.x + b4.x);
-  o4[1] = (__bf16)((v.y - m) * rs * g4.y + b4.y);
-  o4[2] = (__bf16)((v.z - m) * rs * g4.z + b4.z);
-  o4[3] = (__bf16)((v.w - m) * rs * g4.w + b4.w);
   *reinterpret_cast<uint2*>(&dst[row * C_ + lane * 4]) = *reinterpret_cast<uint2*>(o4);
 }
 
@@ -773,57 +600,33 @@
   __bf16*   fbT  = (__bf16*)(ws + OFF_FBT);
   __bf16*   qpk  = (__bf16*)(ws + OFF_QPK);
   __bf16*   kpk  = (__bf16*)(ws + OFF_KPK);
+  _Float16* vph  = (_Float16*)(ws + OFF_VPK);
   __bf16*   qdT  = (__bf16*)(ws + OFF_QDT);
   __bf16*   kdT  = (__bf16*)(ws + OFF_KDT);
   float*    qq   = (float*)(ws + OFF_QQ);
   float*    kk   = (float*)(ws + OFF_KK);
-  float*    out  = (float*)d_out;
-
-  bool big = (ws_size >= WS_NEED2);
-
-  lnA_pack<<<dim3(N_ / 32, B_), 256, 0, stream>>>(featA, fanT, ling, linb);
-  packT_kernel<<<dim3(N_ / 64, C_ / 64, B_), 256, 0, stream>>>(featB, fbT);
+  unsigned int* fsd = (unsigned int*)(ws + OFF_FSD);
+  _Float16* partO = (_Float16*)(ws + OFF_PART);
+  float*    statM = (float*)(ws + OFF_STATM);
+  float*    statL = (float*)(ws + OFF_STATL);
+  __bf16*   csLN  = (__bf16*)(ws + OFF_CSLN);
+  __bf16*   cdLN  = (__bf16*)(ws + OFF_CDLN);
+  __bf16*   X1T   = (__bf16*)(ws + OFF_X1T);
+  float*    out   = (float*)d_out;
+
+  prep_kernel<<<dim3(192, B_), 256, 0, stream>>>(featA, featB, fanT, fbT, ling, linb);
   proj_mfma<<<dim3(N_ / 64, C_ / 64, 5 * B_), 256, 0, stream>>>(
-      fanT, fbT, fanT, big ? 1 : 0, qw, qb, kw, kb, vw, vb, qdw, qdb, kdw, kdb);
+      fanT, fbT, fanT, qw, qb, kw, kb, vw, vb, qdw, qdb, kdw, kdb);
   norms_b<<<dim3(N_ / 64, B_), 256, 0, stream>>>(qdT, kdT, qq, kk);
-
-  if (big){
-    _Float16*     vph  = (_Float16*)(ws + OFF_VPK);
-    unsigned int* fsd  = (unsigned int*)(ws + OFF_FSD);
-    _Float16* partO = (_Float16*)(ws + OFF2_PART);
-    float*    statM = (float*)(ws + OFF2_STATM);
-    float*    statL = (float*)(ws + OFF2_STATL);
-    __bf16*   csLN  = (__bf16*)(ws + OFF2_CSLN);
-    __bf16*   cdLN  = (__bf16*)(ws + OFF2_CDLN);
-    __bf16*   X1T   = (__bf16*)(ws + OFF2_X1T);
-    pairdist_mfma<<<dim3(N_ / 64, N_ / 64, B_), 256, 0, stream>>>(
-        qdT, kdT, qq, kk, xyzA, xyzB, fsd);
-    dual_attn3<<<dim3(N_ / 64, H_, B_ * 2), 256, 0, stream>>>(
-        qpk, kpk, vph, fsd, sbw1, sbg, sbb, sbm, sbv, sbw2, sbb2,
-        partO, statM, statL);
-    combine_ln<<<dim3(B_ * N_ / 4, 2), 256, 0, stream>>>(
-        partO, statM, statL, csLN, cdLN, lsg, lsb, ldg, ldb);
-    fusion1_mfma<<<dim3(N_ / 64, (2 * C_) / 64, B_), 256, 0, stream>>>(
-        fanT, csLN, cdLN, X1T, fw1, fbg, fbb, fbm, fbv);
-    fusion2_mfma<<<dim3(N_ / 64, C_ / 64, B_), 256, 0, stream>>>(
-        X1T, fw2, fb2, featA, out);
-  } else {
-    __bf16*   vpk  = (__bf16*)(ws + OFF_VPK);
-    _Float16* fdh  = (_Float16*)(ws + OFF_FDH);
-    float*  ctxsT = (float*)(ws + OFF_CTXS);
-    float*  ctxdT = (float*)(ws + OFF_CTXD);
-    __bf16* csLN  = (__bf16*)(ws + OFF_CSLN);
-    __bf16* cdLN  = (__bf16*)(ws + OFF_CDLN);
-    __bf16* X1T   = (__bf16*)(ws + OFF_X1T);
-    fdist_mfma<<<dim3(N_ / 64, N_ / 64, B_), 256, 0, stream>>>(qdT, kdT, qq, kk, fdh);
-    dual_attn<<<dim3(N_ / 64, H_, B_), 256, 0, stream>>>(
-        qpk, kpk, vpk, fdh, xyzA, xyzB,
-        sbw1, sbg, sbb, sbm, sbv, sbw2, sbb2, ctxsT, ctxdT);
-    ln_ctx<<<dim3(B_ * N_ / 4, 2), 256, 0, stream>>>(
-        ctxsT, ctxdT, csLN, cdLN, lsg, lsb, ldg, ldb);
-    fusion1_mfma<<<dim3(N_ / 64, (2 * C_) / 64, B_), 256, 0, stream>>>(
-        fanT, csLN, cdLN, X1T, fw1, fbg, fbb, fbm, fbv);
-    fusion2_mfma<<<dim3(N_ / 64, C_ / 64, B_), 256, 0, stream>>>(
-        X1T, fw2, fb2, featA, out);
-  }
-}
+  pairdist_mfma<<<dim3(N_ / 64, N_ / 64, B_), 256, 0, stream>>>(
+      qdT, kdT, qq, kk, xyzA, xyzB, fsd);
+  dual_attn4<<<dim3(N_ / 64, H_, B_ * 2), 256, 0, stream>>>(
+      qpk, kpk, vph, fsd, sbw1, sbg, sbb, sbm, sbv, sbw2, sbb2,
+      partO, statM, statL);
+  combine_ln<<<dim3(B_ * N_ / 4, 2), 256, 0, stream>>>(
+      partO, statM, statL, csLN, cdLN, lsg, lsb, ldg, ldb);
+  fusion1_mfma<<<dim3(N_ / 64, (2 * C_) / 64, B_), 256, 0, stream>>>(
+      fanT, csLN, cdLN, X1T, fw1, fbg, fbb, fbm, fbv);
+  fusion2_mfma<<<dim3(N_ / 64, C_ / 64, B_), 256, 0, stream>>>(
+      X1T, fw2, fb2, featA, out);
+}
```

Result: no change. 265.9 us (-1.8%).
